# Performance work log

Measured on AMD Instinct MI355X. Metric: run time of the kernel, lower is better.

## Reference

```python
import jax, jax.numpy as jnp
import numpy as np
from jax import lax


def _spectral_topk_filter(X, k):
    # X: complex (B, Freq, F). Keep top-k magnitude freqs per (batch, feature).
    Xt = jnp.transpose(X, (0, 2, 1))  # (B, F, Freq)
    mag = jnp.abs(Xt)
    _, idx = lax.top_k(mag, k)  # (B, F, k)
    vals = jnp.take_along_axis(Xt, idx, axis=-1)
    B, F, _ = Xt.shape
    bi = jnp.arange(B)[:, None, None]
    fi = jnp.arange(F)[None, :, None]
    filt = jnp.zeros_like(Xt).at[bi, fi, idx].set(vals)
    return jnp.transpose(filt, (0, 2, 1))  # (B, Freq, F)


def _hamming_periodic(W):
    # matches torch.hamming_window(W) default (periodic=True)
    n = jnp.arange(W, dtype=jnp.float32)
    return 0.54 - 0.46 * jnp.cos(2.0 * jnp.pi * n / W)


def setup_inputs() -> dict:
    key = jax.random.key(0)
    x = jax.random.normal(key, (32, 4096, 128), dtype=jnp.float32)
    return {"x": x, "window_size": 25, "k": 16}


def reference(x, window_size, k):
    B, T, F = x.shape
    W = window_size
    half = W // 2

    # spectral filter: rfft -> keep top-k freqs -> irfft
    X = jnp.fft.rfft(x, axis=1)
    Xf = _spectral_topk_filter(X, k)
    xf = jnp.fft.irfft(Xf, axis=1).astype(x.dtype)  # (B, T, F)

    # flip-padding as in the torch module
    left = xf[:, :half, :][:, ::-1, :]
    right = xf[:, -half:, :][:, ::-1, :]
    xp = jnp.concatenate([left, xf, right], axis=1)  # (B, T + 2*half, F)

    # sliding hamming-window average == depthwise 1D correlation (no kernel flip,
    # matching the elementwise multiply in the original loop)
    w = _hamming_periodic(W).astype(x.dtype)
    xr = jnp.transpose(xp, (0, 2, 1)).reshape(B * F, 1, -1)  # (B*F, 1, Tp)
    out = lax.conv_general_dilated(xr, w[None, None, :], (1,), 'VALID')  # (B*F, 1, T)
    out = out.reshape(B, F, T).transpose(0, 2, 1) / jnp.sum(w)
    return out
```

## Files before the change

kernel.cpp:

```cpp
#include <hip/hip_runtime.h>
#include <math.h>


#define NN     4096
#define LOGN   12
#define NT     256
#define EPT    16
#define KTOP   16
#define WSZ    25
#define HALFW  12
#define FDIM   128
#define BATCH  32
#define TWO_PI 6.283185307179586f

__device__ __forceinline__ int swz(int a) { return a + (a >> 5); }

#define CMUL(r, i, wr_, wi_) { float _r = (r); (r) = _r * (wr_) - (i) * (wi_); (i) = _r * (wi_) + (i) * (wr_); }
#define MULNI(r, i)          { float _r = (r); (r) = (i); (i) = -_r; }

__device__ __forceinline__ void cs_phase(int ph, float& c, float& s)
{
    const float rev = (float)ph * (1.0f / (float)NN);
    s = __builtin_amdgcn_sinf(rev);
    c = __builtin_amdgcn_cosf(rev);
}

__device__ __forceinline__ void dft16(float (&zr)[16], float (&zi)[16])
{
    const float C1 = 0.92387953251128674f;
    const float S1 = 0.38268343236508978f;
    const float R2 = 0.70710678118654752f;
    float yr[16], yi[16];
    #pragma unroll
    for (int n2 = 0; n2 < 4; ++n2) {
        float ar = zr[n2],      ai = zi[n2];
        float br = zr[4 + n2],  bi = zi[4 + n2];
        float cr = zr[8 + n2],  ci = zi[8 + n2];
        float dr = zr[12 + n2], di = zi[12 + n2];
        float t0r = ar + cr, t0i = ai + ci;
        float t1r = ar - cr, t1i = ai - ci;
        float t2r = br + dr, t2i = bi + di;
        float t3r = br - dr, t3i = bi - di;
        yr[n2]      = t0r + t2r;  yi[n2]      = t0i + t2i;
        yr[4 + n2]  = t1r + t3i;  yi[4 + n2]  = t1i - t3r;
        yr[8 + n2]  = t0r - t2r;  yi[8 + n2]  = t0i - t2i;
        yr[12 + n2] = t1r - t3i;  yi[12 + n2] = t1i + t3r;
    }
    CMUL(yr[5],  yi[5],  C1, -S1);
    CMUL(yr[6],  yi[6],  R2, -R2);
    CMUL(yr[7],  yi[7],  S1, -C1);
    CMUL(yr[9],  yi[9],  R2, -R2);
    MULNI(yr[10], yi[10]);
    CMUL(yr[11], yi[11], -R2, -R2);
    CMUL(yr[13], yi[13], S1, -C1);
    CMUL(yr[14], yi[14], -R2, -R2);
    CMUL(yr[15], yi[15], -C1, S1);
    #pragma unroll
    for (int k1 = 0; k1 < 4; ++k1) {
        float ar = yr[k1 * 4 + 0], ai = yi[k1 * 4 + 0];
        float br = yr[k1 * 4 + 1], bi = yi[k1 * 4 + 1];
        float cr = yr[k1 * 4 + 2], ci = yi[k1 * 4 + 2];
        float dr = yr[k1 * 4 + 3], di = yi[k1 * 4 + 3];
        float t0r = ar + cr, t0i = ai + ci;
        float t1r = ar - cr, t1i = ai - ci;
        float t2r = br + dr, t2i = bi + di;
        float t3r = br - dr, t3i = bi - di;
        zr[k1]      = t0r + t2r;  zi[k1]      = t0i + t2i;
        zr[4 + k1]  = t1r + t3i;  zi[4 + k1]  = t1i - t3r;
        zr[8 + k1]  = t0r - t2r;  zi[8 + k1]  = t0i - t2i;
        zr[12 + k1] = t1r - t3i;  zi[12 + k1] = t1i + t3r;
    }
}

__global__ __launch_bounds__(256)
void transpose_kernel(const float* __restrict__ in, float* __restrict__ out,
                      int R, int C)
{
    __shared__ float tile[64][65];
    const int b = blockIdx.z;
    const float* pin  = in  + (size_t)b * R * C;
    float*       pout = out + (size_t)b * R * C;
    const int r0 = blockIdx.y * 64, c0 = blockIdx.x * 64;
    const int tc4 = (threadIdx.x & 15) * 4;
    const int tr  = threadIdx.x >> 4;
    #pragma unroll
    for (int i = 0; i < 4; ++i) {
        int r = tr + i * 16;
        float4 v = *(const float4*)&pin[(size_t)(r0 + r) * C + c0 + tc4];
        tile[r][tc4 + 0] = v.x; tile[r][tc4 + 1] = v.y;
        tile[r][tc4 + 2] = v.z; tile[r][tc4 + 3] = v.w;
    }
    __syncthreads();
    #pragma unroll
    for (int i = 0; i < 4; ++i) {
        int r = tr + i * 16;
        float4 v;
        v.x = tile[tc4 + 0][r]; v.y = tile[tc4 + 1][r];
        v.z = tile[tc4 + 2][r]; v.w = tile[tc4 + 3][r];
        *(float4*)&pout[(size_t)(c0 + r) * R + r0 + tc4] = v;
    }
}

__global__ __launch_bounds__(NT, 4)
void spectral_fft_kernel(float* __restrict__ ws)
{
    __shared__ float s_re[NN + (NN >> 5)];
    __shared__ float s_im[NN + (NN >> 5)];
    __shared__ float s_w[WSZ];
    __shared__ float s_wsum;
    __shared__ float s_rv[8];
    __shared__ int   s_rk[8];
    __shared__ int   s_kf[KTOP];
    __shared__ float s_kr[KTOP];
    __shared__ float s_ki[KTOP];
    __shared__ float s_vr[KTOP];
    __shared__ float s_vi[KTOP];
    __shared__ float s_cd2[KTOP];
    __shared__ float s_edge[2 * HALFW];

    const int tid = threadIdx.x;
    float* chan = ws + (size_t)blockIdx.x * NN;

    if (tid < WSZ)
        s_w[tid] = 0.54f - 0.46f * cosf(TWO_PI * (float)tid / (float)WSZ);

    float zr[16], zi[16];
    #pragma unroll
    for (int r = 0; r < 16; ++r) { zr[r] = chan[tid + (r << 8)]; zi[r] = 0.0f; }

    dft16(zr, zi);

    if (tid == 0) {
        float a = 0.0f;
        for (int i = 0; i < WSZ; ++i) a += s_w[i];
        s_wsum = a;
    }

    {
        float sn, cs;
        sincosf(-TWO_PI * (float)tid / (float)NN, &sn, &cs);
        float dr = cs, di = sn;
        float wr = dr, wi = di;
        #pragma unroll
        for (int u = 1; u < 16; ++u) {
            CMUL(zr[u], zi[u], wr, wi);
            float nr = wr * dr - wi * di; wi = wr * di + wi * dr; wr = nr;
        }
        #pragma unroll
        for (int u = 0; u < 16; ++u) {
            int a = swz(tid + (u << 8));
            s_re[a] = zr[u]; s_im[a] = zi[u];
        }
    }
    __syncthreads();

    {
        const int p = tid & 15;
        const int b0 = ((tid >> 4) << 8) + p;
        #pragma unroll
        for (int r = 0; r < 16; ++r) {
            int a = swz(b0 + (r << 4));
            zr[r] = s_re[a]; zi[r] = s_im[a];
        }
        dft16(zr, zi);
        float sn, cs;
        sincosf(-TWO_PI * (float)(p << 4) / (float)NN, &sn, &cs);
        float dr = cs, di = sn;
        float wr = dr, wi = di;
        #pragma unroll
        for (int u = 1; u < 16; ++u) {
            CMUL(zr[u], zi[u], wr, wi);
            float nr = wr * dr - wi * di; wi = wr * di + wi * dr; wr = nr;
        }
        #pragma unroll
        for (int u = 0; u < 16; ++u) {
            int a = swz(b0 + (u << 4));
            s_re[a] = zr[u]; s_im[a] = zi[u];
        }
    }
    __syncthreads();

    {
        #pragma unroll
        for (int r = 0; r < 16; ++r) {
            int a = swz((tid << 4) + r);
            zr[r] = s_re[a]; zi[r] = s_im[a];
        }
        dft16(zr, zi);
    }

    const int fbase = ((tid & 15) << 4) | (tid >> 4);
    float mg[9];
    float lmax = -1.0f; int lk = 0x7fffffff;
    #pragma unroll
    for (int u = 0; u < 9; ++u) {
        float v = zr[u] * zr[u] + zi[u] * zi[u];
        if (u == 8 && fbase != 0) v = -1.0f;
        mg[u] = v;
        if (v > lmax) { lmax = v; lk = (u << 8) + fbase; }
    }

    for (int r = 0; r < KTOP; ++r) {
        float bv = lmax; int bk = lk;
        #pragma unroll
        for (int off = 32; off > 0; off >>= 1) {
            float ov = __shfl_down(bv, off);
            int   ok = __shfl_down(bk, off);
            if (ov > bv || (ov == bv && ok < bk)) { bv = ov; bk = ok; }
        }
        const int buf = (r & 1) << 2;
        if ((tid & 63) == 0) { s_rv[buf + (tid >> 6)] = bv; s_rk[buf + (tid >> 6)] = bk; }
        __syncthreads();
        bv = s_rv[buf]; bk = s_rk[buf];
        #pragma unroll
        for (int w2 = 1; w2 < 4; ++w2) {
            float ov = s_rv[buf + w2]; int ok = s_rk[buf + w2];
            if (ov > bv || (ov == bv && ok < bk)) { bv = ov; bk = ok; }
        }
        if (lmax == bv && lk == bk) {
            const int uw = bk >> 8;
            s_kf[r] = bk;
            #pragma unroll
            for (int u2 = 0; u2 < 9; ++u2) {
                if (u2 == uw) { s_kr[r] = zr[u2]; s_ki[r] = zi[u2]; mg[u2] = -1.0f; }
            }
            lmax = -1.0f; lk = 0x7fffffff;
            #pragma unroll
            for (int u2 = 0; u2 < 9; ++u2) {
                float v = mg[u2];
                if (v > lmax) { lmax = v; lk = (u2 << 8) + fbase; }
            }
        }
    }
    __syncthreads();

    if (tid < 2 * HALFW) {
        const int te = (tid < HALFW) ? tid : (NN - 2 * HALFW + tid);
        float a = 0.0f;
        for (int r = 0; r < KTOP; ++r) {
            const int fj = s_kf[r];
            float vr = s_kr[r], vi = s_ki[r];
            if (fj == 0 || fj == NN / 2) { vi = 0.0f; }
            else { vr *= 2.0f; vi *= 2.0f; }
            float c, s;
            cs_phase((fj * te) & (NN - 1), c, s);
            a += vr * c - vi * s;
        }
        s_edge[tid] = a * (1.0f / (float)NN);
    }
    if (tid >= 64 && tid < 64 + KTOP) {
        const int r = tid - 64;
        const int fj = s_kf[r];
        float vr = s_kr[r], vi = s_ki[r];
        float sc;
        if (fj == 0 || fj == NN / 2) { vi = 0.0f; sc = 1.0f; }
        else                         { sc = 2.0f; }
        float cr, ci, dc, ds;
        cs_phase((-HALFW * fj) & (NN - 1), cr, ci);
        cs_phase(fj, dc, ds);
        float hr = 0.0f, hi = 0.0f;
        for (int i = 0; i < WSZ; ++i) {
            const float wv = s_w[i];
            hr += wv * cr; hi += wv * ci;
            float nc = cr * dc - ci * ds;
            ci = ci * dc + cr * ds;
            cr = nc;
        }
        const float scale = sc / ((float)NN * s_wsum);
        s_vr[r]  = (vr * hr - vi * hi) * scale;
        s_vi[r]  = (vr * hi + vi * hr) * scale;
        s_cd2[r] = dc + dc;
    }
    __syncthreads();

    const int t0 = tid * EPT;
    float acc[EPT];
    #pragma unroll
    for (int t = 0; t < EPT; ++t) acc[t] = 0.0f;

    for (int r = 0; r < KTOP; ++r) {
        const int fj = s_kf[r];
        const float vr = s_vr[r], vi = s_vi[r];
        const float cd2 = s_cd2[r];
        const int p0 = (fj * t0) & (NN - 1);
        float c0, s0, cm, sm;
        cs_phase(p0, c0, s0);
        cs_phase((p0 - fj) & (NN - 1), cm, sm);
        float g1 = vr * c0 - vi * s0;
        float g0 = vr * cm - vi * sm;
        #pragma unroll
        for (int t = 0; t < EPT; ++t) {
            acc[t] += g1;
            const float gn = __builtin_fmaf(cd2, g1, -g0);
            g0 = g1; g1 = gn;
        }
    }

    if (tid == 0) {
        const float rinv = 1.0f / s_wsum;
        for (int t = 0; t < HALFW; ++t) {
            float d = 0.0f;
            for (int i = 0; t + i < HALFW; ++i)
                d += s_w[i] * (s_edge[HALFW - 1 - t - i] - s_edge[HALFW + t + i]);
            acc[t] += d * rinv;
        }
    }
    if (tid == NT - 1) {
        const float rinv = 1.0f / s_wsum;
        for (int j = 0; j < HALFW; ++j) {
            float d = 0.0f;
            for (int i = 2 * HALFW - j; i < WSZ; ++i)
                d += s_w[i] * (s_edge[4 * HALFW - 1 - j - i] - s_edge[j + i - 2 * HALFW]);
            acc[(EPT - HALFW) + j] += d * rinv;
        }
    }

    #pragma unroll
    for (int t = 0; t < EPT; ++t) s_im[swz(t0 + t)] = acc[t];
    __syncthreads();

    float4* ch4w = (float4*)chan;
    #pragma unroll
    for (int i = 0; i < 4; ++i) {
        int a  = (tid + i * NT) * 4;
        int sa = swz(a);
        float4 v = { s_im[sa], s_im[sa + 1], s_im[sa + 2], s_im[sa + 3] };
        ch4w[tid + i * NT] = v;
    }
}

__global__ __launch_bounds__(NT, 3)
void spectral_filter_fallback(const float* __restrict__ x, float* __restrict__ out)
{
    __shared__ float s_re[NN + (NN >> 5)];
    __shared__ float s_im[NN];
    __shared__ float s_tw[NN];
    __shared__ float s_w[WSZ];
    __shared__ float s_wsum;
    __shared__ float s_rv[NT / 64];
    __shared__ int   s_ri[NT / 64];
    __shared__ int   s_kf[KTOP];
    __shared__ float s_kr[KTOP];
    __shared__ float s_ki[KTOP];

    const int tid = threadIdx.x;
    const int c   = blockIdx.x;
    const int b   = c >> 7;
    const int f   = c & (FDIM - 1);
    const size_t base = (size_t)b * NN * FDIM + f;

    if (tid < WSZ)
        s_w[tid] = 0.54f - 0.46f * cosf(TWO_PI * (float)tid / (float)WSZ);

    for (int i = tid; i < NN / 2; i += NT) {
        float sn, cs;
        sincosf(-TWO_PI * (float)i / (float)NN, &sn, &cs);
        s_tw[i]          = cs;
        s_tw[i + NN / 2] = sn;
    }

    #pragma unroll
    for (int i = 0; i < EPT; ++i) {
        int j = tid + i * NT;
        int t = (int)(__brev((unsigned)j) >> (32 - LOGN));
        s_re[j] = x[base + (size_t)t * FDIM];
        s_im[j] = 0.0f;
    }
    __syncthreads();

    if (tid == 0) {
        float a = 0.0f;
        for (int i = 0; i < WSZ; ++i) a += s_w[i];
        s_wsum = a;
    }

    for (int s = 1; s <= LOGN; ++s) {
        const int half = 1 << (s - 1);
        const int tsh  = LOGN - s;
        #pragma unroll
        for (int i = 0; i < EPT / 2; ++i) {
            int j  = tid + i * NT;
            int p  = j & (half - 1);
            int i0 = ((j >> (s - 1)) << s) + p;
            int i1 = i0 + half;
            int q  = p << tsh;
            float wr = s_tw[q], wi = s_tw[q + NN / 2];
            float ar = s_re[i0], ai = s_im[i0];
            float br = s_re[i1], bi = s_im[i1];
            float tr = br * wr - bi * wi;
            float ti = br * wi + bi * wr;
            s_re[i0] = ar + tr;  s_im[i0] = ai + ti;
            s_re[i1] = ar - tr;  s_im[i1] = ai - ti;
        }
        __syncthreads();
    }

    for (int i = tid; i < NN / 2 + 1; i += NT) {
        float rr = s_re[i], ii = s_im[i];
        s_tw[i] = rr * rr + ii * ii;
    }
    __syncthreads();

    for (int r = 0; r < KTOP; ++r) {
        float best = -1.0f; int bidx = 0x7fffffff;
        for (int i = tid; i < NN / 2 + 1; i += NT) {
            float v = s_tw[i];
            if (v > best) { best = v; bidx = i; }
        }
        #pragma unroll
        for (int off = 32; off > 0; off >>= 1) {
            float ov = __shfl_down(best, off);
            int   oi = __shfl_down(bidx, off);
            if (ov > best || (ov == best && oi < bidx)) { best = ov; bidx = oi; }
        }
        const int wid = tid >> 6;
        if ((tid & 63) == 0) { s_rv[wid] = best; s_ri[wid] = bidx; }
        __syncthreads();
        if (tid == 0) {
            float bv = s_rv[0]; int bx = s_ri[0];
            #pragma unroll
            for (int w2 = 1; w2 < NT / 64; ++w2) {
                float ov = s_rv[w2]; int oi = s_ri[w2];
                if (ov > bv || (ov == bv && oi < bx)) { bv = ov; bx = oi; }
            }
            s_kf[r] = bx;
            s_kr[r] = s_re[bx];
            s_ki[r] = s_im[bx];
            s_tw[bx] = -1.0f;
        }
        __syncthreads();
    }

    const int t0 = tid * EPT;
    float xf[EPT];
    #pragma unroll
    for (int i = 0; i < EPT; ++i) xf[i] = 0.0f;

    for (int r = 0; r < KTOP; ++r) {
        const int fj = s_kf[r];
        float vr = s_kr[r], vi = s_ki[r];
        float sc = 2.0f;
        if (fj == 0 || fj == NN / 2) { sc = 1.0f; vi = 0.0f; }
        vr *= sc; vi *= sc;
        const int ph0 = (fj * t0) & (NN - 1);
        float c0, s0, dc, ds;
        sincosf((float)ph0 * (TWO_PI / (float)NN), &s0, &c0);
        sincosf((float)fj  * (TWO_PI / (float)NN), &ds, &dc);
        float cr = c0, ci = s0;
        #pragma unroll
        for (int i = 0; i < EPT; ++i) {
            xf[i] += vr * cr - vi * ci;
            float nc = cr * dc - ci * ds;
            ci = ci * dc + cr * ds;
            cr = nc;
        }
    }
    __syncthreads();

    #pragma unroll
    for (int i = 0; i < EPT; ++i)
        s_re[swz(t0 + i)] = xf[i] * (1.0f / (float)NN);
    __syncthreads();

    float win[EPT + WSZ - 1];
    #pragma unroll
    for (int i = 0; i < EPT + WSZ - 1; ++i) {
        int a = t0 + i - HALFW;
        if (a < 0)        a = -1 - a;
        else if (a >= NN) a = 2 * NN - 1 - a;
        win[i] = s_re[swz(a)];
    }

    const float rinv = 1.0f / s_wsum;
    float acc[EPT];
    #pragma unroll
    for (int t = 0; t < EPT; ++t) acc[t] = 0.0f;
    #pragma unroll
    for (int i = 0; i < WSZ; ++i) {
        const float wv = s_w[i];
        #pragma unroll
        for (int t = 0; t < EPT; ++t) acc[t] += win[t + i] * wv;
    }
    #pragma unroll
    for (int t = 0; t < EPT; ++t)
        out[base + (size_t)(t0 + t) * FDIM] = acc[t] * rinv;
}

extern "C" void kernel_launch(void* const* d_in, const int* in_sizes, int n_in,
                              void* d_out, int out_size, void* d_ws, size_t ws_size,
                              hipStream_t stream)
{
    const float* x = (const float*)d_in[0];
    float* out = (float*)d_out;
    const size_t need = (size_t)BATCH * FDIM * NN * sizeof(float);
    if (ws_size >= need) {
        float* ws = (float*)d_ws;
        transpose_kernel<<<dim3(FDIM / 64, NN / 64, BATCH), 256, 0, stream>>>(x, ws, NN, FDIM);
        spectral_fft_kernel<<<dim3(BATCH * FDIM), NT, 0, stream>>>(ws);
        transpose_kernel<<<dim3(NN / 64, FDIM / 64, BATCH), 256, 0, stream>>>(ws, out, FDIM, NN);
    } else {
        spectral_filter_fallback<<<dim3(BATCH * FDIM), NT, 0, stream>>>(x, out);
    }
}
```

Baseline: 254.1 us.

## Fuse reconstruction with output transpose via compact per-channel spectral records

```diff
diff --git a/kernel.cpp b/kernel.cpp
--- a/kernel.cpp
+++ b/kernel.cpp
@@ -11,6 +11,8 @@
 #define HALFW  12
 #define FDIM   128
 #define BATCH  32
+#define RECL   88
+#define TT     128
 #define TWO_PI 6.283185307179586f
 
 __device__ __forceinline__ int swz(int a) { return a + (a >> 5); }
@@ -117,6 +119,7 @@
     __shared__ float s_vi[KTOP];
     __shared__ float s_cd2[KTOP];
     __shared__ float s_edge[2 * HALFW];
+    __shared__ float s_dl[2 * HALFW];
 
     const int tid = threadIdx.x;
     float* chan = ws + (size_t)blockIdx.x * NN;
@@ -273,59 +276,102 @@
     }
     __syncthreads();
 
-    const int t0 = tid * EPT;
-    float acc[EPT];
-    #pragma unroll
-    for (int t = 0; t < EPT; ++t) acc[t] = 0.0f;
-
-    for (int r = 0; r < KTOP; ++r) {
-        const int fj = s_kf[r];
-        const float vr = s_vr[r], vi = s_vi[r];
-        const float cd2 = s_cd2[r];
-        const int p0 = (fj * t0) & (NN - 1);
-        float c0, s0, cm, sm;
-        cs_phase(p0, c0, s0);
-        cs_phase((p0 - fj) & (NN - 1), cm, sm);
-        float g1 = vr * c0 - vi * s0;
-        float g0 = vr * cm - vi * sm;
-        #pragma unroll
-        for (int t = 0; t < EPT; ++t) {
-            acc[t] += g1;
-            const float gn = __builtin_fmaf(cd2, g1, -g0);
-            g0 = g1; g1 = gn;
-        }
-    }
-
     if (tid == 0) {
         const float rinv = 1.0f / s_wsum;
         for (int t = 0; t < HALFW; ++t) {
             float d = 0.0f;
             for (int i = 0; t + i < HALFW; ++i)
                 d += s_w[i] * (s_edge[HALFW - 1 - t - i] - s_edge[HALFW + t + i]);
-            acc[t] += d * rinv;
-        }
-    }
-    if (tid == NT - 1) {
-        const float rinv = 1.0f / s_wsum;
+            s_dl[t] = d * rinv;
+        }
         for (int j = 0; j < HALFW; ++j) {
             float d = 0.0f;
             for (int i = 2 * HALFW - j; i < WSZ; ++i)
                 d += s_w[i] * (s_edge[4 * HALFW - 1 - j - i] - s_edge[j + i - 2 * HALFW]);
-            acc[(EPT - HALFW) + j] += d * rinv;
-        }
-    }
-
-    #pragma unroll
-    for (int t = 0; t < EPT; ++t) s_im[swz(t0 + t)] = acc[t];
-    __syncthreads();
-
-    float4* ch4w = (float4*)chan;
-    #pragma unroll
-    for (int i = 0; i < 4; ++i) {
-        int a  = (tid + i * NT) * 4;
-        int sa = swz(a);
-        float4 v = { s_im[sa], s_im[sa + 1], s_im[sa + 2], s_im[sa + 3] };
-        ch4w[tid + i * NT] = v;
+            s_dl[HALFW + j] = d * rinv;
+        }
+    }
+    __syncthreads();
+
+    if (tid < RECL) {
+        float v;
+        if      (tid < 16) v = s_vr[tid];
+        else if (tid < 32) v = s_vi[tid - 16];
+        else if (tid < 48) v = s_cd2[tid - 32];
+        else if (tid < 64) v = (float)s_kf[tid - 48];
+        else               v = s_dl[tid - 64];
+        chan[tid] = v;
+    }
+}
+
+__global__ __launch_bounds__(NT, 3)
+void spectral_recon_kernel(const float* __restrict__ ws, float* __restrict__ out)
+{
+    __shared__ float s_c[FDIM * (RECL + 1)];
+
+    const int tid = threadIdx.x;
+    const int tb  = blockIdx.x * TT;
+    const int b   = blockIdx.y;
+    const int chB = b * FDIM;
+
+    #pragma unroll
+    for (int k = 0; k < (FDIM * RECL) / NT; ++k) {
+        int idx = tid + k * NT;
+        int ch  = idx / RECL;
+        int j   = idx - ch * RECL;
+        s_c[ch * (RECL + 1) + j] = ws[(size_t)(chB + ch) * NN + j];
+    }
+    __syncthreads();
+
+    const int m  = tid & 31;
+    const int tq = tid >> 5;
+    const int t0 = tb + tq * 16;
+
+    float acc[4][16];
+    #pragma unroll
+    for (int c = 0; c < 4; ++c)
+        #pragma unroll
+        for (int i = 0; i < 16; ++i) acc[c][i] = 0.0f;
+
+    for (int r = 0; r < KTOP; ++r) {
+        #pragma unroll
+        for (int c = 0; c < 4; ++c) {
+            const float* rec = &s_c[(c * 32 + m) * (RECL + 1)];
+            const float vr  = rec[r];
+            const float vi  = rec[16 + r];
+            const float cd2 = rec[32 + r];
+            const int   fj  = (int)rec[48 + r];
+            const int   p0  = (fj * t0) & (NN - 1);
+            float c0, s0, cm, sm;
+            cs_phase(p0, c0, s0);
+            cs_phase((p0 - fj) & (NN - 1), cm, sm);
+            float g1 = vr * c0 - vi * s0;
+            float g0 = vr * cm - vi * sm;
+            #pragma unroll
+            for (int i = 0; i < 16; ++i) {
+                acc[c][i] += g1;
+                const float gn = __builtin_fmaf(cd2, g1, -g0);
+                g0 = g1; g1 = gn;
+            }
+        }
+    }
+
+    #pragma unroll
+    for (int c = 0; c < 4; ++c) {
+        const int ch = c * 32 + m;
+        const float* rec = &s_c[ch * (RECL + 1)];
+        if (tb == 0 && tq == 0) {
+            #pragma unroll
+            for (int i = 0; i < HALFW; ++i) acc[c][i] += rec[64 + i];
+        }
+        if (tb == NN - TT && tq == 7) {
+            #pragma unroll
+            for (int i = 4; i < 16; ++i) acc[c][i] += rec[76 + (i - 4)];
+        }
+        const size_t obase = ((size_t)b * NN + t0) * FDIM + ch;
+        #pragma unroll
+        for (int i = 0; i < 16; ++i)
+            out[obase + (size_t)i * FDIM] = acc[c][i];
     }
 }
 
@@ -497,7 +543,7 @@
         float* ws = (float*)d_ws;
         transpose_kernel<<<dim3(FDIM / 64, NN / 64, BATCH), 256, 0, stream>>>(x, ws, NN, FDIM);
         spectral_fft_kernel<<<dim3(BATCH * FDIM), NT, 0, stream>>>(ws);
-        transpose_kernel<<<dim3(NN / 64, FDIM / 64, BATCH), 256, 0, stream>>>(ws, out, FDIM, NN);
+        spectral_recon_kernel<<<dim3(NN / TT, BATCH), NT, 0, stream>>>(ws, out);
     } else {
         spectral_filter_fallback<<<dim3(BATCH * FDIM), NT, 0, stream>>>(x, out);
     }
```

Measured after the change: 248.6 us. 1.02x faster.
